# Kernel tuning notes

Measured on AMD Instinct MI355X. Metric: run time of the kernel, lower is better.

The kernel has to match this reference:

```python
import jax, jax.numpy as jnp
import numpy as np

DS_STEPS = 9
MAX_RND = 1.0
SMOKE_AUG = 0.5
SIZE = 512


def diamond_square(key, steps=DS_STEPS, max_rnd=MAX_RND):
    """Vectorized, faithful port of f_seed_grid + f_dsmain.

    Notes on faithfulness to the original code:
      - interior 'temp' reads in the diamond step resolve to the cell's own
        center (i_min + half == i_mid), exactly as in the original (buggy)
        indexing, so the interior averages double-count the center.
      - the '== 0' guards mean top/left edge midpoints are only written for
        the first row/column of cells (fresh zeros); elsewhere they were
        already written as bottom/right edges of neighboring cells.
    All per-level updates read only square-step (center) and coarser-level
    values, so each level is fully parallel.
    """
    N = 2 ** steps + 1
    hm = jnp.zeros((N, N), jnp.float32)
    corners = jax.random.uniform(jax.random.fold_in(key, 1000), (4,), minval=-1.0, maxval=1.0)
    hm = (hm.at[0, 0].set(corners[0]).at[0, -1].set(corners[1])
            .at[-1, 0].set(corners[2]).at[-1, -1].set(corners[3]))
    L = N - 1  # shape_length
    for level in range(steps):
        g = 2 ** level          # grid_split
        h = L // 2              # half_v_grid_size
        r = max_rnd / (level + 1)
        ks = jax.random.split(jax.random.fold_in(key, level), 5)
        lows = jnp.arange(g) * L
        highs = lows + L
        mids = lows + h
        # corner reads (set at coarser levels / seeds)
        nw = hm[lows[:, None], lows[None, :]]
        ne = hm[lows[:, None], highs[None, :]]
        sw = hm[highs[:, None], lows[None, :]]
        se = hm[highs[:, None], highs[None, :]]
        # square step: cell centers
        centers = (nw + ne + sw + se) / 4.0 + jax.random.uniform(ks[0], (g, g), minval=-r, maxval=r)
        hm = hm.at[mids[:, None], mids[None, :]].set(centers)
        # diamond step (all reads from post-square values)
        # top row (only i_min==0 cells pass the ==0 guard); temp = hm[max_index-h, j_mid] = centers[g-1, j]
        top = (centers[0, :] + hm[0, lows] + hm[0, highs] + centers[g - 1, :]) / 4.0 \
              + jax.random.uniform(ks[1], (g,), minval=-r, maxval=r)
        # left col (only j_min==0 cells); temp = hm[i_mid, max_index-h] = centers[i, g-1]
        left = (centers[:, 0] + hm[lows, 0] + hm[highs, 0] + centers[:, g - 1]) / 4.0 \
               + jax.random.uniform(ks[2], (g,), minval=-r, maxval=r)
        # right edges of every cell; interior temp == own center, boundary temp = centers[i, 0]
        temp_r = jnp.where(jnp.arange(g)[None, :] < g - 1, centers, centers[:, :1])
        right = (centers + ne + se + temp_r) / 4.0 + jax.random.uniform(ks[3], (g, g), minval=-r, maxval=r)
        # bottom edges of every cell; interior temp == own center, boundary temp = centers[0, j]
        temp_b = jnp.where(jnp.arange(g)[:, None] < g - 1, centers, centers[:1, :])
        bottom = (centers + sw + se + temp_b) / 4.0 + jax.random.uniform(ks[4], (g, g), minval=-r, maxval=r)
        hm = hm.at[0, mids].set(top)
        hm = hm.at[mids, 0].set(left)
        hm = hm.at[mids[:, None], highs[None, :]].set(right)
        hm = hm.at[highs[:, None], mids[None, :]].set(bottom)
        L //= 2
    return hm


def make_smoke_noise(key):
    hm = diamond_square(key)
    noise = (hm - hm.min()) / (hm.max() - hm.min())          # [513, 513] in [0,1]
    noise = jax.image.resize(noise, (SIZE, SIZE), method="bilinear")
    return noise * SMOKE_AUG                                  # [H, W]


def setup_inputs() -> dict:
    key = jax.random.key(0)
    img = jax.random.uniform(key, (32, 3, 512, 512), dtype=jnp.float32)
    return {"img": img}


def reference(img) -> jnp.ndarray:
    rn = make_smoke_noise(jax.random.key(42))                 # [H, W]
    rn = rn[None, None]                                       # broadcast over [B, C, H, W]
    return jnp.clip(img * (1.0 - rn) + rn, 0.0, 1.0)
```

## Files before the change

kernel.cpp:

```cpp
#include <hip/hip_runtime.h>

struct KP { unsigned a, b; };

__host__ __device__ constexpr unsigned rotl32(unsigned x, int d) {
  return (x << d) | (x >> (32 - d));
}

__host__ __device__ constexpr KP tf2x32(unsigned k0, unsigned k1, unsigned x0, unsigned x1) {
  unsigned k2 = k0 ^ k1 ^ 0x1BD11BDAu;
  unsigned v0 = x0 + k0;
  unsigned v1 = x1 + k1;
  const int R[5][4] = {{13,15,26,6},{17,29,16,24},{13,15,26,6},{17,29,16,24},{13,15,26,6}};
  const unsigned KI[5][2] = {{k1, k2 + 1u},{k2, k0 + 2u},{k0, k1 + 3u},{k1, k2 + 4u},{k2, k0 + 5u}};
  for (int g = 0; g < 5; ++g) {
    for (int r = 0; r < 4; ++r) {
      v0 += v1;
      v1 = rotl32(v1, R[g][r]);
      v1 ^= v0;
    }
    v0 += KI[g][0];
    v1 += KI[g][1];
  }
  return KP{v0, v1};
}

struct AllKeys {
  unsigned lk[9][5][2];
  unsigned ck[2];
};

__host__ __device__ constexpr AllKeys make_keys() {
  AllKeys K{};
  for (int l = 0; l < 9; ++l) {
    KP base = tf2x32(0u, 42u, 0u, (unsigned)l);
    for (int m = 0; m < 5; ++m) {
      KP s = tf2x32(base.a, base.b, 0u, (unsigned)m);
      K.lk[l][m][0] = s.a;
      K.lk[l][m][1] = s.b;
    }
  }
  KP ck = tf2x32(0u, 42u, 0u, 1000u);
  K.ck[0] = ck.a;
  K.ck[1] = ck.b;
  return K;
}

constexpr AllKeys KEYS = make_keys();

#define NG 513

__device__ inline unsigned rbits(unsigned k0, unsigned k1, unsigned i) {
  KP o = tf2x32(k0, k1, 0u, i);
  return o.a ^ o.b;
}

__device__ inline float bits_to_u(unsigned b, float r) {
  float u = __uint_as_float((b >> 9) | 0x3f800000u) - 1.0f;
  return fmaxf(-r, u * (2.0f * r) - r);
}

__device__ inline float draw_u(const unsigned* kk, unsigned i, float r) {
  return bits_to_u(rbits(kk[0], kk[1], i), r);
}

__device__ inline float cell_center(const float* hm, int level, int g, int L,
                                    int a, int b, float r) {
  int lo_i = a * L, hi_i = lo_i + L, lo_j = b * L, hi_j = lo_j + L;
  float nw = hm[lo_i * NG + lo_j], ne = hm[lo_i * NG + hi_j];
  float sw = hm[hi_i * NG + lo_j], se = hm[hi_i * NG + hi_j];
  return (nw + ne + sw + se) * 0.25f +
         draw_u(KEYS.lk[level][0], (unsigned)(a * g + b), r);
}

__device__ inline void do_cell(float* hm, int level, int i, int j) {
  int g = 1 << level;
  int L = 512 >> level;
  int h = L >> 1;
  float r = 1.0f / (float)(level + 1);
  int lo_i = i * L, hi_i = lo_i + L, mi_i = lo_i + h;
  int lo_j = j * L, hi_j = lo_j + L, mi_j = lo_j + h;
  float nw = hm[lo_i * NG + lo_j], ne = hm[lo_i * NG + hi_j];
  float sw = hm[hi_i * NG + lo_j], se = hm[hi_i * NG + hi_j];
  unsigned m = (unsigned)(i * g + j);

  float c = (nw + ne + sw + se) * 0.25f + draw_u(KEYS.lk[level][0], m, r);
  hm[mi_i * NG + mi_j] = c;

  float tr = (j < g - 1) ? c : cell_center(hm, level, g, L, i, 0, r);
  float right = (c + ne + se + tr) * 0.25f + draw_u(KEYS.lk[level][3], m, r);
  hm[mi_i * NG + hi_j] = right;

  float tb = (i < g - 1) ? c : cell_center(hm, level, g, L, 0, j, r);
  float bottom = (c + sw + se + tb) * 0.25f + draw_u(KEYS.lk[level][4], m, r);
  hm[hi_i * NG + mi_j] = bottom;

  if (i == 0) {
    float cg1 = (g == 1) ? c : cell_center(hm, level, g, L, g - 1, j, r);
    float top = (c + hm[lo_j] + hm[hi_j] + cg1) * 0.25f +
                draw_u(KEYS.lk[level][1], (unsigned)j, r);
    hm[mi_j] = top;
  }
  if (j == 0) {
    float cg1 = (g == 1) ? c : cell_center(hm, level, g, L, i, g - 1, r);
    float left = (c + hm[lo_i * NG] + hm[hi_i * NG] + cg1) * 0.25f +
                 draw_u(KEYS.lk[level][2], (unsigned)i, r);
    hm[mi_i * NG] = left;
  }
}

__global__ void k_ds_small(float* hm, unsigned* mmx) {
  int tid = threadIdx.x;
  if (tid == 0) {
#pragma unroll
    for (int q = 0; q < 4; ++q) {
      float v = bits_to_u(rbits(KEYS.ck[0], KEYS.ck[1], (unsigned)q), 1.0f);
      int y = (q >> 1) ? 512 : 0;
      int x = (q & 1) ? 512 : 0;
      hm[y * NG + x] = v;
    }
    mmx[0] = 0xFFFFFFFFu;
    mmx[1] = 0u;
  }
  __syncthreads();
  for (int lvl = 0; lvl <= 5; ++lvl) {
    int g = 1 << lvl;
    if (tid < g * g) do_cell(hm, lvl, tid >> lvl, tid & (g - 1));
    __syncthreads();
  }
}

__global__ void k_level(float* hm, int level) {
  int g = 1 << level;
  int gt = blockIdx.x * blockDim.x + threadIdx.x;
  do_cell(hm, level, gt >> level, gt & (g - 1));
}

__device__ inline unsigned enc_f(float f) {
  unsigned u = __float_as_uint(f);
  return (u & 0x80000000u) ? ~u : (u | 0x80000000u);
}
__device__ inline float dec_f(unsigned e) {
  unsigned u = (e & 0x80000000u) ? (e & 0x7FFFFFFFu) : ~e;
  return __uint_as_float(u);
}

__global__ void k_minmax(const float* hm, unsigned* mmx) {
  int gtid = blockIdx.x * blockDim.x + threadIdx.x;
  int nthreads = gridDim.x * blockDim.x;
  float mn = 3.4e38f, mx = -3.4e38f;
  for (int idx = gtid; idx < NG * NG; idx += nthreads) {
    float v = hm[idx];
    mn = fminf(mn, v);
    mx = fmaxf(mx, v);
  }
#pragma unroll
  for (int off = 32; off >= 1; off >>= 1) {
    mn = fminf(mn, __shfl_down(mn, off, 64));
    mx = fmaxf(mx, __shfl_down(mx, off, 64));
  }
  if ((threadIdx.x & 63) == 0) {
    atomicMin(&mmx[0], enc_f(mn));
    atomicMax(&mmx[1], enc_f(mx));
  }
}

__global__ void k_noise(const float* hm, const unsigned* mmx, float* rn) {
  int o = blockIdx.x * blockDim.x + threadIdx.x;
  int oy = o >> 9, ox = o & 511;
  const float csc = 512.0f / 513.0f;
  float dx = (float)(2 * ox + 1) * (1.0f / 1024.0f);
  float wx0 = 1.0f - dx * csc;
  float wx1 = 1.0f - (1.0f - dx) * csc;
  float sx = wx0 + wx1;
  wx0 /= sx; wx1 /= sx;
  float dy = (float)(2 * oy + 1) * (1.0f / 1024.0f);
  float wy0 = 1.0f - dy * csc;
  float wy1 = 1.0f - (1.0f - dy) * csc;
  float sy = wy0 + wy1;
  wy0 /= sy; wy1 /= sy;
  const float* r0 = hm + oy * NG + ox;
  float v = wy0 * (wx0 * r0[0] + wx1 * r0[1]) + wy1 * (wx0 * r0[NG] + wx1 * r0[NG + 1]);
  float mn = dec_f(mmx[0]), mx = dec_f(mmx[1]);
  rn[o] = 0.5f * ((v - mn) / (mx - mn));
}

__global__ void k_apply(const float4* __restrict__ img, const float* __restrict__ rn,
                        float4* __restrict__ out) {
  int t = blockIdx.x * blockDim.x + threadIdx.x;
  int pos4 = t & ((512 * 512 / 4) - 1);
  float4 a = img[t];
  float4 n = reinterpret_cast<const float4*>(rn)[pos4];
  float4 o;
  o.x = fminf(fmaxf(a.x * (1.0f - n.x) + n.x, 0.0f), 1.0f);
  o.y = fminf(fmaxf(a.y * (1.0f - n.y) + n.y, 0.0f), 1.0f);
  o.z = fminf(fmaxf(a.z * (1.0f - n.z) + n.z, 0.0f), 1.0f);
  o.w = fminf(fmaxf(a.w * (1.0f - n.w) + n.w, 0.0f), 1.0f);
  out[t] = o;
}

__global__ void k_apply_direct(const float* __restrict__ img, const float* __restrict__ hm,
                               const unsigned* __restrict__ mmx, float* __restrict__ out) {
  int t = blockIdx.x * blockDim.x + threadIdx.x;
  int pos = t & (512 * 512 - 1);
  int oy = pos >> 9, ox = pos & 511;
  const float csc = 512.0f / 513.0f;
  float dx = (float)(2 * ox + 1) * (1.0f / 1024.0f);
  float wx0 = 1.0f - dx * csc;
  float wx1 = 1.0f - (1.0f - dx) * csc;
  float sx = wx0 + wx1;
  wx0 /= sx; wx1 /= sx;
  float dy = (float)(2 * oy + 1) * (1.0f / 1024.0f);
  float wy0 = 1.0f - dy * csc;
  float wy1 = 1.0f - (1.0f - dy) * csc;
  float sy = wy0 + wy1;
  wy0 /= sy; wy1 /= sy;
  const float* r0 = hm + oy * NG + ox;
  float v = wy0 * (wx0 * r0[0] + wx1 * r0[1]) + wy1 * (wx0 * r0[NG] + wx1 * r0[NG + 1]);
  float mn = dec_f(mmx[0]), mx = dec_f(mmx[1]);
  float rnv = 0.5f * ((v - mn) / (mx - mn));
  float a = img[t];
  out[t] = fminf(fmaxf(a * (1.0f - rnv) + rnv, 0.0f), 1.0f);
}

extern "C" void kernel_launch(void* const* d_in, const int* in_sizes, int n_in,
                              void* d_out, int out_size, void* d_ws, size_t ws_size,
                              hipStream_t stream) {
  const float* img = (const float*)d_in[0];
  float* out = (float*)d_out;
  unsigned char* ws = (unsigned char*)d_ws;

  const size_t RN_BYTES = 512 * 512 * sizeof(float);
  const size_t HM_BYTES = NG * NG * sizeof(float);
  const size_t need_full = 16 + RN_BYTES + HM_BYTES;

  unsigned* mmx = (unsigned*)ws;
  bool use_rn = (ws_size >= need_full);
  float* rn = (float*)(ws + 16);
  float* hm = use_rn ? (float*)(ws + 16 + RN_BYTES) : (float*)(ws + 16);

  hipLaunchKernelGGL(k_ds_small, dim3(1), dim3(1024), 0, stream, hm, mmx);
  hipLaunchKernelGGL(k_level, dim3(16), dim3(256), 0, stream, hm, 6);
  hipLaunchKernelGGL(k_level, dim3(64), dim3(256), 0, stream, hm, 7);
  hipLaunchKernelGGL(k_level, dim3(256), dim3(256), 0, stream, hm, 8);
  hipLaunchKernelGGL(k_minmax, dim3(64), dim3(256), 0, stream, hm, mmx);

  const int total = 32 * 3 * 512 * 512;
  if (use_rn) {
    hipLaunchKernelGGL(k_noise, dim3(512 * 512 / 256), dim3(256), 0, stream, hm, mmx, rn);
    hipLaunchKernelGGL(k_apply, dim3(total / 4 / 256), dim3(256), 0, stream,
                       (const float4*)img, rn, (float4*)out);
  } else {
    hipLaunchKernelGGL(k_apply_direct, dim3(total / 256), dim3(256), 0, stream,
                       img, hm, mmx, out);
  }
}
```

Baseline: 219.6 us.

## Fuse diamond-square levels into cooperative kernel and fuse noise into apply

Replaces the chain of per-level diamond-square launches and the min/max kernel with a single cooperative kernel that uses grid-wide syncs between levels. The noise-map kernel is folded into the apply kernel, so each thread computes four bilinear noise values once and reuses them across 24 image planes. This removes several launches and the intermediate noise buffer round trip. The cost is a cooperative launch with grid syncs and an apply grid of only 256 blocks, each thread looping over many planes, which may reduce memory-level parallelism.

```diff
diff --git a/kernel.cpp b/kernel.cpp
--- a/kernel.cpp
+++ b/kernel.cpp
@@ -1,4 +1,7 @@
 #include <hip/hip_runtime.h>
+#include <hip/hip_cooperative_groups.h>
+
+namespace cg = cooperative_groups;
 
 struct KP { unsigned a, b; };
 
@@ -108,6 +111,69 @@
   }
 }
 
+__device__ inline unsigned enc_f(float f) {
+  unsigned u = __float_as_uint(f);
+  return (u & 0x80000000u) ? ~u : (u | 0x80000000u);
+}
+__device__ inline float dec_f(unsigned e) {
+  unsigned u = (e & 0x80000000u) ? (e & 0x7FFFFFFFu) : ~e;
+  return __uint_as_float(u);
+}
+
+__global__ void __launch_bounds__(256) k_ds_coop(float* hm, unsigned* mmx) {
+  cg::grid_group grid = cg::this_grid();
+  const int tid = threadIdx.x;
+  const int gtid = blockIdx.x * 256 + tid;
+
+  if (blockIdx.x == 0) {
+    if (tid == 0) {
+#pragma unroll
+      for (int q = 0; q < 4; ++q) {
+        float v = bits_to_u(rbits(KEYS.ck[0], KEYS.ck[1], (unsigned)q), 1.0f);
+        int y = (q >> 1) ? 512 : 0;
+        int x = (q & 1) ? 512 : 0;
+        hm[y * NG + x] = v;
+      }
+      mmx[0] = 0xFFFFFFFFu;
+      mmx[1] = 0u;
+    }
+    __syncthreads();
+    for (int lvl = 0; lvl <= 5; ++lvl) {
+      int g = 1 << lvl;
+      for (int c = tid; c < g * g; c += 256)
+        do_cell(hm, lvl, c >> lvl, c & (g - 1));
+      __syncthreads();
+    }
+  }
+  __threadfence();
+  grid.sync();
+  if (gtid < 4096) do_cell(hm, 6, gtid >> 6, gtid & 63);
+  __threadfence();
+  grid.sync();
+  if (gtid < 16384) do_cell(hm, 7, gtid >> 7, gtid & 127);
+  __threadfence();
+  grid.sync();
+  do_cell(hm, 8, gtid >> 8, gtid & 255);
+  __threadfence();
+  grid.sync();
+
+  float mn = 3.4e38f, mx = -3.4e38f;
+  for (int idx = gtid; idx < NG * NG; idx += 256 * 256) {
+    float v = hm[idx];
+    mn = fminf(mn, v);
+    mx = fmaxf(mx, v);
+  }
+#pragma unroll
+  for (int off = 32; off >= 1; off >>= 1) {
+    mn = fminf(mn, __shfl_down(mn, off, 64));
+    mx = fmaxf(mx, __shfl_down(mx, off, 64));
+  }
+  if ((tid & 63) == 0) {
+    atomicMin(&mmx[0], enc_f(mn));
+    atomicMax(&mmx[1], enc_f(mx));
+  }
+}
+
 __global__ void k_ds_small(float* hm, unsigned* mmx) {
   int tid = threadIdx.x;
   if (tid == 0) {
@@ -135,15 +201,6 @@
   do_cell(hm, level, gt >> level, gt & (g - 1));
 }
 
-__device__ inline unsigned enc_f(float f) {
-  unsigned u = __float_as_uint(f);
-  return (u & 0x80000000u) ? ~u : (u | 0x80000000u);
-}
-__device__ inline float dec_f(unsigned e) {
-  unsigned u = (e & 0x80000000u) ? (e & 0x7FFFFFFFu) : ~e;
-  return __uint_as_float(u);
-}
-
 __global__ void k_minmax(const float* hm, unsigned* mmx) {
   int gtid = blockIdx.x * blockDim.x + threadIdx.x;
   int nthreads = gridDim.x * blockDim.x;
@@ -164,62 +221,72 @@
   }
 }
 
-__global__ void k_noise(const float* hm, const unsigned* mmx, float* rn) {
-  int o = blockIdx.x * blockDim.x + threadIdx.x;
-  int oy = o >> 9, ox = o & 511;
+__global__ void __launch_bounds__(1024) k_apply_fused(
+    const float4* __restrict__ img, const float* __restrict__ hm,
+    const unsigned* __restrict__ mmx, float4* __restrict__ out) {
+  int t = blockIdx.x * 1024 + threadIdx.x;
+  int pos4 = t & 65535;
+  int pg = t >> 16;
+  int oy = pos4 >> 7;
+  int ox = (pos4 & 127) << 2;
+
   const float csc = 512.0f / 513.0f;
-  float dx = (float)(2 * ox + 1) * (1.0f / 1024.0f);
-  float wx0 = 1.0f - dx * csc;
-  float wx1 = 1.0f - (1.0f - dx) * csc;
-  float sx = wx0 + wx1;
-  wx0 /= sx; wx1 /= sx;
   float dy = (float)(2 * oy + 1) * (1.0f / 1024.0f);
   float wy0 = 1.0f - dy * csc;
   float wy1 = 1.0f - (1.0f - dy) * csc;
   float sy = wy0 + wy1;
   wy0 /= sy; wy1 /= sy;
+
   const float* r0 = hm + oy * NG + ox;
-  float v = wy0 * (wx0 * r0[0] + wx1 * r0[1]) + wy1 * (wx0 * r0[NG] + wx1 * r0[NG + 1]);
+  const float* r1 = r0 + NG;
+  float a0 = r0[0], a1 = r0[1], a2 = r0[2], a3 = r0[3], a4 = r0[4];
+  float b0 = r1[0], b1 = r1[1], b2 = r1[2], b3 = r1[3], b4 = r1[4];
+
   float mn = dec_f(mmx[0]), mx = dec_f(mmx[1]);
-  rn[o] = 0.5f * ((v - mn) / (mx - mn));
-}
-
-__global__ void k_apply(const float4* __restrict__ img, const float* __restrict__ rn,
-                        float4* __restrict__ out) {
-  int t = blockIdx.x * blockDim.x + threadIdx.x;
-  int pos4 = t & ((512 * 512 / 4) - 1);
-  float4 a = img[t];
-  float4 n = reinterpret_cast<const float4*>(rn)[pos4];
-  float4 o;
-  o.x = fminf(fmaxf(a.x * (1.0f - n.x) + n.x, 0.0f), 1.0f);
-  o.y = fminf(fmaxf(a.y * (1.0f - n.y) + n.y, 0.0f), 1.0f);
-  o.z = fminf(fmaxf(a.z * (1.0f - n.z) + n.z, 0.0f), 1.0f);
-  o.w = fminf(fmaxf(a.w * (1.0f - n.w) + n.w, 0.0f), 1.0f);
-  out[t] = o;
-}
-
-__global__ void k_apply_direct(const float* __restrict__ img, const float* __restrict__ hm,
-                               const unsigned* __restrict__ mmx, float* __restrict__ out) {
-  int t = blockIdx.x * blockDim.x + threadIdx.x;
-  int pos = t & (512 * 512 - 1);
-  int oy = pos >> 9, ox = pos & 511;
-  const float csc = 512.0f / 513.0f;
-  float dx = (float)(2 * ox + 1) * (1.0f / 1024.0f);
-  float wx0 = 1.0f - dx * csc;
-  float wx1 = 1.0f - (1.0f - dx) * csc;
-  float sx = wx0 + wx1;
-  wx0 /= sx; wx1 /= sx;
-  float dy = (float)(2 * oy + 1) * (1.0f / 1024.0f);
-  float wy0 = 1.0f - dy * csc;
-  float wy1 = 1.0f - (1.0f - dy) * csc;
-  float sy = wy0 + wy1;
-  wy0 /= sy; wy1 /= sy;
-  const float* r0 = hm + oy * NG + ox;
-  float v = wy0 * (wx0 * r0[0] + wx1 * r0[1]) + wy1 * (wx0 * r0[NG] + wx1 * r0[NG + 1]);
-  float mn = dec_f(mmx[0]), mx = dec_f(mmx[1]);
-  float rnv = 0.5f * ((v - mn) / (mx - mn));
-  float a = img[t];
-  out[t] = fminf(fmaxf(a * (1.0f - rnv) + rnv, 0.0f), 1.0f);
+
+  float4 n;
+  {
+    float dx = (float)(2 * ox + 1) * (1.0f / 1024.0f);
+    float wx0 = 1.0f - dx * csc, wx1 = 1.0f - (1.0f - dx) * csc;
+    float sx = wx0 + wx1; wx0 /= sx; wx1 /= sx;
+    float v = wy0 * (wx0 * a0 + wx1 * a1) + wy1 * (wx0 * b0 + wx1 * b1);
+    n.x = 0.5f * ((v - mn) / (mx - mn));
+  }
+  {
+    float dx = (float)(2 * (ox + 1) + 1) * (1.0f / 1024.0f);
+    float wx0 = 1.0f - dx * csc, wx1 = 1.0f - (1.0f - dx) * csc;
+    float sx = wx0 + wx1; wx0 /= sx; wx1 /= sx;
+    float v = wy0 * (wx0 * a1 + wx1 * a2) + wy1 * (wx0 * b1 + wx1 * b2);
+    n.y = 0.5f * ((v - mn) / (mx - mn));
+  }
+  {
+    float dx = (float)(2 * (ox + 2) + 1) * (1.0f / 1024.0f);
+    float wx0 = 1.0f - dx * csc, wx1 = 1.0f - (1.0f - dx) * csc;
+    float sx = wx0 + wx1; wx0 /= sx; wx1 /= sx;
+    float v = wy0 * (wx0 * a2 + wx1 * a3) + wy1 * (wx0 * b2 + wx1 * b3);
+    n.z = 0.5f * ((v - mn) / (mx - mn));
+  }
+  {
+    float dx = (float)(2 * (ox + 3) + 1) * (1.0f / 1024.0f);
+    float wx0 = 1.0f - dx * csc, wx1 = 1.0f - (1.0f - dx) * csc;
+    float sx = wx0 + wx1; wx0 /= sx; wx1 /= sx;
+    float v = wy0 * (wx0 * a3 + wx1 * a4) + wy1 * (wx0 * b3 + wx1 * b4);
+    n.w = 0.5f * ((v - mn) / (mx - mn));
+  }
+  float4 cn;
+  cn.x = 1.0f - n.x; cn.y = 1.0f - n.y; cn.z = 1.0f - n.z; cn.w = 1.0f - n.w;
+
+  int base = pg * (24 * 65536) + pos4;
+#pragma unroll 4
+  for (int p = 0; p < 24; ++p) {
+    float4 a = img[base + p * 65536];
+    float4 o;
+    o.x = fminf(fmaxf(a.x * cn.x + n.x, 0.0f), 1.0f);
+    o.y = fminf(fmaxf(a.y * cn.y + n.y, 0.0f), 1.0f);
+    o.z = fminf(fmaxf(a.z * cn.z + n.z, 0.0f), 1.0f);
+    o.w = fminf(fmaxf(a.w * cn.w + n.w, 0.0f), 1.0f);
+    out[base + p * 65536] = o;
+  }
 }
 
 extern "C" void kernel_launch(void* const* d_in, const int* in_sizes, int n_in,
@@ -229,28 +296,20 @@
   float* out = (float*)d_out;
   unsigned char* ws = (unsigned char*)d_ws;
 
-  const size_t RN_BYTES = 512 * 512 * sizeof(float);
-  const size_t HM_BYTES = NG * NG * sizeof(float);
-  const size_t need_full = 16 + RN_BYTES + HM_BYTES;
-
   unsigned* mmx = (unsigned*)ws;
-  bool use_rn = (ws_size >= need_full);
-  float* rn = (float*)(ws + 16);
-  float* hm = use_rn ? (float*)(ws + 16 + RN_BYTES) : (float*)(ws + 16);
-
-  hipLaunchKernelGGL(k_ds_small, dim3(1), dim3(1024), 0, stream, hm, mmx);
-  hipLaunchKernelGGL(k_level, dim3(16), dim3(256), 0, stream, hm, 6);
-  hipLaunchKernelGGL(k_level, dim3(64), dim3(256), 0, stream, hm, 7);
-  hipLaunchKernelGGL(k_level, dim3(256), dim3(256), 0, stream, hm, 8);
-  hipLaunchKernelGGL(k_minmax, dim3(64), dim3(256), 0, stream, hm, mmx);
-
-  const int total = 32 * 3 * 512 * 512;
-  if (use_rn) {
-    hipLaunchKernelGGL(k_noise, dim3(512 * 512 / 256), dim3(256), 0, stream, hm, mmx, rn);
-    hipLaunchKernelGGL(k_apply, dim3(total / 4 / 256), dim3(256), 0, stream,
-                       (const float4*)img, rn, (float4*)out);
-  } else {
-    hipLaunchKernelGGL(k_apply_direct, dim3(total / 256), dim3(256), 0, stream,
-                       img, hm, mmx, out);
-  }
-}
+  float* hm = (float*)(ws + 16);
+
+  void* args[] = {(void*)&hm, (void*)&mmx};
+  hipError_t e = hipLaunchCooperativeKernel((const void*)k_ds_coop, dim3(256),
+                                            dim3(256), args, 0, stream);
+  if (e != hipSuccess) {
+    hipLaunchKernelGGL(k_ds_small, dim3(1), dim3(1024), 0, stream, hm, mmx);
+    hipLaunchKernelGGL(k_level, dim3(16), dim3(256), 0, stream, hm, 6);
+    hipLaunchKernelGGL(k_level, dim3(64), dim3(256), 0, stream, hm, 7);
+    hipLaunchKernelGGL(k_level, dim3(256), dim3(256), 0, stream, hm, 8);
+    hipLaunchKernelGGL(k_minmax, dim3(64), dim3(256), 0, stream, hm, mmx);
+  }
+
+  hipLaunchKernelGGL(k_apply_fused, dim3(256), dim3(1024), 0, stream,
+                     (const float4*)img, hm, mmx, (float4*)out);
+}
```

Measured after the change: 455.4 us. +107.3%, slower.
